# Kernel optimization log

Measured on AMD Instinct MI355X. Metric: run time of the kernel, lower is better.

The kernel has to match this reference:

```python
import jax, jax.numpy as jnp
import numpy as np

H = 64; H2 = 32; B = 256; NPART = 64
NP = B * NPART          # 16384 part nodes
PER_TF = 512            # torque/force nodes per graph
NT = B * PER_TF; NF = NT
E = 262144              # edges per edge type
L = 5; T = 4            # 4 main hetero layers + 1 actor layer; 4 edge types
NEG = 0.2; EPS = 1e-5


def _seg_softmax(e, seg, n):
    # softmax over entries sharing the same segment id (along axis 0)
    m = jax.lax.stop_gradient(jax.ops.segment_max(e, seg, num_segments=n))
    ex = jnp.exp(e - m[seg])
    s = jax.ops.segment_sum(ex, seg, num_segments=n)
    return ex / s[seg]


def _gat(x_s, x_d, es, ed, Ws, Wd, a_s, a_d, b, n_dst):
    # PyG GATConv, heads=1, add_self_loops=False, bipartite (x_src, x_dst)
    hs = x_s @ Ws                      # [Ns,H]
    hd = x_d @ Wd                      # [Nd,H]
    e = jax.nn.leaky_relu((hs @ a_s)[es] + (hd @ a_d)[ed], NEG)   # [E]
    al = _seg_softmax(e, ed, n_dst)                                # attn per dst neighborhood
    return jax.ops.segment_sum(al[:, None] * hs[es], ed, num_segments=n_dst) + b


def _hetero_layer(xp, xt, xf, edges, Ws, Wd, a_s, a_d, b):
    # to_hetero(aggr='sum'): one GATConv per edge type, sum into each dst type
    (pts, ptd), (tps, tpd), (pfs, pfd), (fps, fpd) = edges
    out_t = _gat(xp, xt, pts, ptd, Ws[0], Wd[0], a_s[0], a_d[0], b[0], xt.shape[0])
    out_p = (_gat(xt, xp, tps, tpd, Ws[1], Wd[1], a_s[1], a_d[1], b[1], xp.shape[0])
             + _gat(xf, xp, fps, fpd, Ws[3], Wd[3], a_s[3], a_d[3], b[3], xp.shape[0]))
    out_f = _gat(xp, xf, pfs, pfd, Ws[2], Wd[2], a_s[2], a_d[2], b[2], xf.shape[0])
    return out_p, out_t, out_f


def _pool(x):
    # MultiAggregation([max, min, mean]); segments are uniform -> reshape
    xr = x.reshape(B, -1, x.shape[-1])
    return jnp.concatenate([xr.max(1), xr.min(1), xr.mean(1)], axis=-1)


def reference(mass, part_state, torque_x, force_x,
              e_pt_src, e_pt_dst, e_tp_src, e_tp_dst,
              e_pf_src, e_pf_dst, e_fp_src, e_fp_dst,
              batch, part_id,
              emb_parts_W, emb_state, W_src, W_dst, a_src, a_dst, b_conv,
              ln_gamma, ln_beta, out_a_W, out_a_b,
              innet_W, innet_b, full_W, full_b, outnet_W, outnet_b):
    edges = ((e_pt_src, e_pt_dst), (e_tp_src, e_tp_dst),
             (e_pf_src, e_pf_dst), (e_fp_src, e_fp_dst))
    idx = part_state[:, 0] + 2 * part_state[:, 1]
    xp = jnp.concatenate([mass @ emb_parts_W, emb_state[idx]], axis=-1)  # [NP,H]
    xt, xf = torque_x, force_x
    for l in range(4):  # main hetero GAT, ReLU between layers, none after last
        xp, xt, xf = _hetero_layer(xp, xt, xf, edges,
                                   W_src[l], W_dst[l], a_src[l], a_dst[l], b_conv[l])
        if l < 3:
            xp, xt, xf = jax.nn.relu(xp), jax.nn.relu(xt), jax.nn.relu(xf)
    # actor: 1-layer hetero GAT (no activation)
    ap, at, af = _hetero_layer(xp, xt, xf, edges,
                               W_src[4], W_dst[4], a_src[4], a_dst[4], b_conv[4])
    # node LayerNorm
    mu = ap.mean(-1, keepdims=True)
    var = ((ap - mu) ** 2).mean(-1, keepdims=True)
    ra = (ap - mu) / jnp.sqrt(var + EPS) * ln_gamma + ln_beta
    ra = ra @ out_a_W + out_a_b                         # [NP,2]
    soft = _seg_softmax(ra, batch, B)                   # softmax per graph, per channel
    actions = jnp.zeros((B, 2, NPART), dtype=ra.dtype).at[batch, :, part_id].set(soft)
    actions = actions.reshape(B, 2 * NPART)
    rep = jnp.concatenate([_pool(xp), _pool(xt), _pool(xf)], axis=1)   # [B, 9H]
    repV = jax.nn.gelu(rep @ innet_W + innet_b, approximate=False)
    repV = jax.nn.gelu(repV @ full_W + full_b, approximate=False)
    V = jnp.tanh(repV @ outnet_W + outnet_b)            # [B,1]
    return actions, V


def setup_inputs():
    key = jax.random.key(0)
    ks = iter(jax.random.split(key, 40))
    f32 = jnp.float32
    inp = {}
    inp['mass'] = jax.random.uniform(next(ks), (NP, 1), dtype=f32)
    inp['part_state'] = jax.random.randint(next(ks), (NP, 2), 0, 2, dtype=jnp.int32)
    inp['torque_x'] = jax.random.normal(next(ks), (NT, H), dtype=f32)
    inp['force_x'] = jax.random.normal(next(ks), (NF, H), dtype=f32)
    for name, n in [('e_pt_src', NP), ('e_pt_dst', NT), ('e_tp_src', NT), ('e_tp_dst', NP),
                    ('e_pf_src', NP), ('e_pf_dst', NF), ('e_fp_src', NF), ('e_fp_dst', NP)]:
        inp[name] = jax.random.randint(next(ks), (E,), 0, n, dtype=jnp.int32)
    inp['batch'] = (jnp.arange(NP) // NPART).astype(jnp.int32)
    inp['part_id'] = (jnp.arange(NP) % NPART).astype(jnp.int32)
    s = 1.0 / np.sqrt(H)
    inp['emb_parts_W'] = jax.random.normal(next(ks), (1, H2), dtype=f32)
    inp['emb_state'] = jax.random.normal(next(ks), (4, H2), dtype=f32)
    inp['W_src'] = jax.random.normal(next(ks), (L, T, H, H), dtype=f32) * s
    inp['W_dst'] = jax.random.normal(next(ks), (L, T, H, H), dtype=f32) * s
    inp['a_src'] = jax.random.normal(next(ks), (L, T, H), dtype=f32) * s
    inp['a_dst'] = jax.random.normal(next(ks), (L, T, H), dtype=f32) * s
    inp['b_conv'] = jax.random.normal(next(ks), (L, T, H), dtype=f32) * 0.01
    inp['ln_gamma'] = jnp.ones((H,), dtype=f32)
    inp['ln_beta'] = jnp.zeros((H,), dtype=f32)
    inp['out_a_W'] = jax.random.normal(next(ks), (H, 2), dtype=f32) * s
    inp['out_a_b'] = jnp.zeros((2,), dtype=f32)
    inp['innet_W'] = jax.random.normal(next(ks), (9 * H, H), dtype=f32) / np.sqrt(9.0 * H)
    inp['innet_b'] = jnp.zeros((H,), dtype=f32)
    inp['full_W'] = jax.random.normal(next(ks), (H, H), dtype=f32) * s
    inp['full_b'] = jnp.zeros((H,), dtype=f32)
    inp['outnet_W'] = jax.random.normal(next(ks), (H, 1), dtype=f32) * s
    inp['outnet_b'] = jnp.zeros((1,), dtype=f32)
    return inp
```

## Files before the change

kernel.cpp:

```cpp
#include <hip/hip_runtime.h>
#include <math.h>

#define NP_ 16384
#define NT_ 131072
#define NF_ 131072
#define E_  262144
#define B_  256
#define NDTOT 294912
#define E4_  1048576

#define D0 0
#define D1 131072
#define D2 147456
#define D3 278528
#define S0 0
#define S1 16384
#define S2 147456
#define S3 163840

__device__ __forceinline__ float dot4(float4 a, float4 b) {
  return a.x * b.x + a.y * b.y + a.z * b.z + a.w * b.w;
}

__device__ __forceinline__ float4 gather_row(int kb, int ke, float ad,
    const int* __restrict__ sortsrc, const float* __restrict__ aS_seg,
    const float* __restrict__ xsrc, int q, int lanebase, float* si_out) {
  float4 acc = make_float4(0.f, 0.f, 0.f, 0.f);
  float m = -3e38f, ssum = 0.f;
  for (int base = kb; base < ke; base += 16) {
    int k = base + q;
    int valid = (k < ke);
    int sidx = valid ? sortsrc[k] : 0;
    float e = -3e38f;
    if (valid) {
      e = aS_seg[sidx] + ad;
      e = e > 0.f ? e : 0.2f * e;
    }
    float cm = e;
#pragma unroll
    for (int off = 1; off < 16; off <<= 1) cm = fmaxf(cm, __shfl_xor(cm, off));
    float mn = fmaxf(m, cm);
    float w = valid ? __expf(e - mn) : 0.f;
    float ws = w;
#pragma unroll
    for (int off = 1; off < 16; off <<= 1) ws += __shfl_xor(ws, off);
    float r = __expf(m - mn);
    ssum = ssum * r + ws;
    acc.x *= r; acc.y *= r; acc.z *= r; acc.w *= r;
    int cnt = min(16, ke - base);
    int i = 0;
    for (; i + 4 <= cnt; i += 4) {
      float w0 = __shfl(w, lanebase + i, 64);
      float w1 = __shfl(w, lanebase + i + 1, 64);
      float w2 = __shfl(w, lanebase + i + 2, 64);
      float w3 = __shfl(w, lanebase + i + 3, 64);
      int s0 = __shfl(sidx, lanebase + i, 64);
      int s1 = __shfl(sidx, lanebase + i + 1, 64);
      int s2 = __shfl(sidx, lanebase + i + 2, 64);
      int s3 = __shfl(sidx, lanebase + i + 3, 64);
      float4 x0 = *(const float4*)(xsrc + (size_t)s0 * 64 + q * 4);
      float4 x1 = *(const float4*)(xsrc + (size_t)s1 * 64 + q * 4);
      float4 x2 = *(const float4*)(xsrc + (size_t)s2 * 64 + q * 4);
      float4 x3 = *(const float4*)(xsrc + (size_t)s3 * 64 + q * 4);
      acc.x += w0 * x0.x + w1 * x1.x + w2 * x2.x + w3 * x3.x;
      acc.y += w0 * x0.y + w1 * x1.y + w2 * x2.y + w3 * x3.y;
      acc.z += w0 * x0.z + w1 * x1.z + w2 * x2.z + w3 * x3.z;
      acc.w += w0 * x0.w + w1 * x1.w + w2 * x2.w + w3 * x3.w;
    }
    for (; i < cnt; i++) {
      float wi = __shfl(w, lanebase + i, 64);
      int si = __shfl(sidx, lanebase + i, 64);
      float4 xv = *(const float4*)(xsrc + (size_t)si * 64 + q * 4);
      acc.x += wi * xv.x; acc.y += wi * xv.y; acc.z += wi * xv.z; acc.w += wi * xv.w;
    }
    m = mn;
  }
  *si_out = (ssum > 0.f) ? 1.f / ssum : 0.f;
  return acc;
}

__global__ void k_wa(const float* __restrict__ Wsrc, const float* __restrict__ Wdst,
                     const float* __restrict__ asrc, const float* __restrict__ adst,
                     float* __restrict__ wsas, float* __restrict__ wdad) {
  int b = blockIdx.x;
  int lt = b >> 1;
  int role = b & 1;
  int k = threadIdx.x;
  const float* W = (role == 0 ? Wsrc : Wdst) + ((size_t)(lt * 64 + k)) * 64;
  const float* a = (role == 0 ? asrc : adst) + lt * 64;
  float s = 0.f;
  for (int i = 0; i < 64; i++) s += W[i] * a[i];
  (role == 0 ? wsas : wdad)[lt * 64 + k] = s;
}

__global__ __launch_bounds__(256) void k_build_xp(const float* __restrict__ mass,
    const int* __restrict__ ps, const float* __restrict__ embW,
    const float* __restrict__ embS, const float* __restrict__ wsas,
    const float* __restrict__ wdad, float* __restrict__ xp,
    float* __restrict__ aS, float* __restrict__ aD) {
  int tid = threadIdx.x;
  int n = blockIdx.x * 16 + (tid >> 4);
  int q = tid & 15;
  float4 v;
  if (q < 8) {
    float mv = mass[n];
    const float* e = embW + q * 4;
    v.x = mv * e[0]; v.y = mv * e[1]; v.z = mv * e[2]; v.w = mv * e[3];
  } else {
    int idx = ps[n * 2] + 2 * ps[n * 2 + 1];
    const float4* e = (const float4*)(embS + idx * 32 + (q - 8) * 4);
    v = *e;
  }
  *(float4*)(xp + (size_t)n * 64 + q * 4) = v;
  float4 w0 = *(const float4*)(wsas + 0 * 64 + q * 4);
  float4 w2 = *(const float4*)(wsas + 2 * 64 + q * 4);
  float4 d1 = *(const float4*)(wdad + 1 * 64 + q * 4);
  float4 d3 = *(const float4*)(wdad + 3 * 64 + q * 4);
  float p0 = dot4(v, w0), p2 = dot4(v, w2), p1 = dot4(v, d1), p3 = dot4(v, d3);
#pragma unroll
  for (int off = 1; off < 16; off <<= 1) {
    p0 += __shfl_xor(p0, off); p2 += __shfl_xor(p2, off);
    p1 += __shfl_xor(p1, off); p3 += __shfl_xor(p3, off);
  }
  if (q == 0) { aS[S0 + n] = p0; aS[S2 + n] = p2; aD[D1 + n] = p1; aD[D3 + n] = p3; }
}

__global__ __launch_bounds__(256) void k_init_dots(const float* __restrict__ tx,
    const float* __restrict__ fx, const float* __restrict__ wsas,
    const float* __restrict__ wdad, float* __restrict__ aS, float* __restrict__ aD) {
  int tid = threadIdx.x;
  int q = tid & 15, slot = tid >> 4;
  int b = blockIdx.x;
  int isF = (b >= 8192);
  int n = (isF ? b - 8192 : b) * 16 + slot;
  const float* src = (isF ? fx : tx) + (size_t)n * 64 + q * 4;
  float4 v = *(const float4*)src;
  int tsrc = isF ? 3 : 1, tdst = isF ? 2 : 0;
  float4 ws = *(const float4*)(wsas + tsrc * 64 + q * 4);
  float4 wd = *(const float4*)(wdad + tdst * 64 + q * 4);
  float pS = dot4(v, ws), pD = dot4(v, wd);
#pragma unroll
  for (int off = 1; off < 16; off <<= 1) {
    pS += __shfl_xor(pS, off); pD += __shfl_xor(pD, off);
  }
  if (q == 0) {
    if (!isF) { aS[S1 + n] = pS; aD[D0 + n] = pD; }
    else      { aS[S3 + n] = pS; aD[D2 + n] = pD; }
  }
}

__global__ __launch_bounds__(256) void k_count(
    const int* __restrict__ d0, const int* __restrict__ d1,
    const int* __restrict__ d2, const int* __restrict__ d3,
    int* __restrict__ counts) {
  __shared__ int cnt[64];
  int b = blockIdx.x;
  int t = b >> 6, c = b & 63;
  const int* dp = (t == 0) ? d0 : (t == 1) ? d1 : (t == 2) ? d2 : d3;
  int sh = (t & 1) ? 8 : 11;
  int tid = threadIdx.x;
  if (tid < 64) cnt[tid] = 0;
  __syncthreads();
  const int4* dp4 = (const int4*)dp + (size_t)c * 1024;
  for (int i = tid; i < 1024; i += 256) {
    int4 v = dp4[i];
    atomicAdd(&cnt[v.x >> sh], 1);
    atomicAdd(&cnt[v.y >> sh], 1);
    atomicAdd(&cnt[v.z >> sh], 1);
    atomicAdd(&cnt[v.w >> sh], 1);
  }
  __syncthreads();
  if (tid < 64) counts[(b << 6) + tid] = cnt[tid];
}

__global__ __launch_bounds__(256) void k_bases(const int* __restrict__ counts,
    int* __restrict__ cbase, int* __restrict__ granBase, int* __restrict__ rowptr) {
  __shared__ int tot[256];
  int tid = threadIdx.x;
  int t = tid >> 6, g = tid & 63;
  int s = 0;
  for (int c = 0; c < 64; c++) s += counts[(((t << 6) | c) << 6) + g];
  tot[tid] = s;
  __syncthreads();
  for (int off = 1; off < 256; off <<= 1) {
    int x = 0; if (tid >= off) x = tot[tid - off];
    __syncthreads(); tot[tid] += x; __syncthreads();
  }
  int gb = tot[tid] - s;
  granBase[tid] = gb;
  if (tid == 255) granBase[256] = E4_;
  if (tid == 0) rowptr[NDTOT] = E4_;
  int run = gb;
  for (int c = 0; c < 64; c++) {
    int idx = (((t << 6) | c) << 6) + g;
    int v = counts[idx];
    cbase[idx] = run;
    run += v;
  }
}

__global__ __launch_bounds__(256) void k_place(
    const int* __restrict__ d0, const int* __restrict__ s0,
    const int* __restrict__ d1, const int* __restrict__ s1,
    const int* __restrict__ d2, const int* __restrict__ s2,
    const int* __restrict__ d3, const int* __restrict__ s3,
    const int* __restrict__ cbase, int2* __restrict__ pairs) {
  __shared__ int cur[64];
  int b = blockIdx.x;
  int t = b >> 6, c = b & 63;
  const int* dp; const int* sp;
  if (t == 0) { dp = d0; sp = s0; }
  else if (t == 1) { dp = d1; sp = s1; }
  else if (t == 2) { dp = d2; sp = s2; }
  else { dp = d3; sp = s3; }
  int sh = (t & 1) ? 8 : 11;
  int tid = threadIdx.x;
  if (tid < 64) cur[tid] = cbase[(b << 6) + tid];
  __syncthreads();
  const int4* dp4 = (const int4*)dp + (size_t)c * 1024;
  const int4* sp4 = (const int4*)sp + (size_t)c * 1024;
  for (int i = tid; i < 1024; i += 256) {
    int4 d = dp4[i];
    int4 s = sp4[i];
    int pos;
    pos = atomicAdd(&cur[d.x >> sh], 1); pairs[pos] = make_int2(d.x, s.x);
    pos = atomicAdd(&cur[d.y >> sh], 1); pairs[pos] = make_int2(d.y, s.y);
    pos = atomicAdd(&cur[d.z >> sh], 1); pairs[pos] = make_int2(d.z, s.z);
    pos = atomicAdd(&cur[d.w >> sh], 1); pairs[pos] = make_int2(d.w, s.w);
  }
}

__global__ __launch_bounds__(256) void k_build(const int2* __restrict__ pairs,
    const int* __restrict__ granBase, int* __restrict__ rowptr,
    int* __restrict__ sortsrc) {
  __shared__ int cnt[2048];
  __shared__ int psum[256];
  int g = blockIdx.x;
  int t = g >> 6, gg = g & 63;
  int rows = (t & 1) ? 256 : 2048;
  int rowLo = gg * rows;
  int csr0;
  if (t == 0) csr0 = D0 + rowLo;
  else if (t == 1) csr0 = D1 + rowLo;
  else if (t == 2) csr0 = D2 + rowLo;
  else csr0 = D3 + rowLo;
  int eb = granBase[g], ee = granBase[g + 1];
  int tid = threadIdx.x;
  for (int i = tid; i < rows; i += 256) cnt[i] = 0;
  __syncthreads();
  for (int i = eb + tid; i < ee; i += 256) {
    int2 p = pairs[i];
    atomicAdd(&cnt[p.x - rowLo], 1);
  }
  __syncthreads();
  int per = rows >> 8;
  int b0 = tid * per;
  int s = 0;
  for (int j = 0; j < per; j++) s += cnt[b0 + j];
  psum[tid] = s;
  __syncthreads();
  for (int off = 1; off < 256; off <<= 1) {
    int x = 0; if (tid >= off) x = psum[tid - off];
    __syncthreads(); psum[tid] += x; __syncthreads();
  }
  int run = psum[tid] - s;
  for (int j = 0; j < per; j++) {
    int v = cnt[b0 + j];
    cnt[b0 + j] = run;
    rowptr[csr0 + b0 + j] = eb + run;
    run += v;
  }
  __syncthreads();
  for (int i = eb + tid; i < ee; i += 256) {
    int2 p = pairs[i];
    int pos = eb + atomicAdd(&cnt[p.x - rowLo], 1);
    sortsrc[pos] = p.y;
  }
}

__global__ __launch_bounds__(256) void k_part_hs(int l, const float* __restrict__ Wsrc,
    const float* __restrict__ bconv, const float* __restrict__ xt,
    const float* __restrict__ xf, const float* __restrict__ xp,
    const int* __restrict__ rowptr, const int* __restrict__ sortsrc,
    const float* __restrict__ aSrd, const float* __restrict__ aDrd,
    float* __restrict__ aSwr, float* __restrict__ aDwr,
    const float* __restrict__ wsas, const float* __restrict__ wdad,
    float* __restrict__ xpo, float* __restrict__ hs0, float* __restrict__ hs2,
    int relu, int writeDots) {
  __shared__ float Wl[4096];
  __shared__ float shC[2176];
  int tid = threadIdx.x;

  if (blockIdx.x >= NP_ / 16) {
    int b = blockIdx.x - NP_ / 16;
    const float4* W0g = (const float4*)(Wsrc + (size_t)(l * 4 + 0) * 4096);
    const float4* W2g = (const float4*)(Wsrc + (size_t)(l * 4 + 2) * 4096);
#pragma unroll
    for (int i = 0; i < 4; i++) ((float4*)Wl)[i * 256 + tid] = W0g[i * 256 + tid];
    int rlocal = tid >> 4, q = tid & 15;
    int n = b * 16 + rlocal;
    float4 xv = *(const float4*)(xp + (size_t)n * 64 + q * 4);
    *(float4*)(shC + rlocal * 68 + q * 4) = xv;
    __syncthreads();
    const float* xr = shC + rlocal * 68;
    const float4* Wc = (const float4*)Wl;
    float4 o0 = make_float4(0.f, 0.f, 0.f, 0.f);
#pragma unroll 4
    for (int k4 = 0; k4 < 16; k4++) {
      float4 a4 = *(const float4*)(xr + k4 * 4);
#pragma unroll
      for (int kk = 0; kk < 4; kk++) {
        float av = kk == 0 ? a4.x : kk == 1 ? a4.y : kk == 2 ? a4.z : a4.w;
        float4 w0 = Wc[(k4 * 4 + kk) * 16 + q];
        o0.x += av * w0.x; o0.y += av * w0.y; o0.z += av * w0.z; o0.w += av * w0.w;
      }
    }
    *(float4*)(hs0 + (size_t)n * 64 + q * 4) = o0;
    __syncthreads();
#pragma unroll
    for (int i = 0; i < 4; i++) ((float4*)Wl)[i * 256 + tid] = W2g[i * 256 + tid];
    __syncthreads();
    float4 o2 = make_float4(0.f, 0.f, 0.f, 0.f);
#pragma unroll 4
    for (int k4 = 0; k4 < 16; k4++) {
      float4 a4 = *(const float4*)(xr + k4 * 4);
#pragma unroll
      for (int kk = 0; kk < 4; kk++) {
        float av = kk == 0 ? a4.x : kk == 1 ? a4.y : kk == 2 ? a4.z : a4.w;
        float4 w2 = Wc[(k4 * 4 + kk) * 16 + q];
        o2.x += av * w2.x; o2.y += av * w2.y; o2.z += av * w2.z; o2.w += av * w2.w;
      }
    }
    *(float4*)(hs2 + (size_t)n * 64 + q * 4) = o2;
    return;
  }

  float* rowA = shC; float* rowB = shC + 1088;
  const float4* W1g = (const float4*)(Wsrc + (size_t)(l * 4 + 1) * 4096);
  const float4* W3g = (const float4*)(Wsrc + (size_t)(l * 4 + 3) * 4096);
#pragma unroll
  for (int i = 0; i < 4; i++) ((float4*)Wl)[i * 256 + tid] = W1g[i * 256 + tid];

  int rlocal = tid >> 4;
  int q = tid & 15;
  int lanebase = (tid & 63) & 48;
  int n = blockIdx.x * 16 + rlocal;
  int row1 = D1 + n;
  int row3 = D3 + n;

  {
    int kb = rowptr[row1], ke = rowptr[row1 + 1];
    float si;
    float4 acc = gather_row(kb, ke, aDrd[row1], sortsrc, aSrd + S1, xt, q, lanebase, &si);
    acc.x *= si; acc.y *= si; acc.z *= si; acc.w *= si;
    *(float4*)(rowA + rlocal * 68 + q * 4) = acc;
  }
  {
    int kb = rowptr[row3], ke = rowptr[row3 + 1];
    float si;
    float4 acc = gather_row(kb, ke, aDrd[row3], sortsrc, aSrd + S3, xf, q, lanebase, &si);
    acc.x *= si; acc.y *= si; acc.z *= si; acc.w *= si;
    *(float4*)(rowB + rlocal * 68 + q * 4) = acc;
  }
  __syncthreads();

  const float* b1 = bconv + (l * 4 + 1) * 64;
  const float* b3 = bconv + (l * 4 + 3) * 64;
  float4 o = *(const float4*)(b1 + q * 4);
  float4 o3b = *(const float4*)(b3 + q * 4);
  o.x += o3b.x; o.y += o3b.y; o.z += o3b.z; o.w += o3b.w;
  const float4* Wc = (const float4*)Wl;
#pragma unroll 4
  for (int k4 = 0; k4 < 16; k4++) {
    float4 a4 = *(const float4*)(rowA + rlocal * 68 + k4 * 4);
#pragma unroll
    for (int kk = 0; kk < 4; kk++) {
      float av = kk == 0 ? a4.x : kk == 1 ? a4.y : kk == 2 ? a4.z : a4.w;
      float4 w1 = Wc[(k4 * 4 + kk) * 16 + q];
      o.x += av * w1.x; o.y += av * w1.y; o.z += av * w1.z; o.w += av * w1.w;
    }
  }
  __syncthreads();
#pragma unroll
  for (int i = 0; i < 4; i++) ((float4*)Wl)[i * 256 + tid] = W3g[i * 256 + tid];
  __syncthreads();
#pragma unroll 4
  for (int k4 = 0; k4 < 16; k4++) {
    float4 b4 = *(const float4*)(rowB + rlocal * 68 + k4 * 4);
#pragma unroll
    for (int kk = 0; kk < 4; kk++) {
      float bv = kk == 0 ? b4.x : kk == 1 ? b4.y : kk == 2 ? b4.z : b4.w;
      float4 w3 = Wc[(k4 * 4 + kk) * 16 + q];
      o.x += bv * w3.x; o.y += bv * w3.y; o.z += bv * w3.z; o.w += bv * w3.w;
    }
  }
  if (relu) { o.x = fmaxf(o.x, 0.f); o.y = fmaxf(o.y, 0.f); o.z = fmaxf(o.z, 0.f); o.w = fmaxf(o.w, 0.f); }
  *(float4*)(xpo + (size_t)n * 64 + q * 4) = o;

  if (writeDots) {
    float4 w0 = *(const float4*)(wsas + (size_t)((l + 1) * 4 + 0) * 64 + q * 4);
    float4 w2 = *(const float4*)(wsas + (size_t)((l + 1) * 4 + 2) * 64 + q * 4);
    float4 d1 = *(const float4*)(wdad + (size_t)((l + 1) * 4 + 1) * 64 + q * 4);
    float4 d3 = *(const float4*)(wdad + (size_t)((l + 1) * 4 + 3) * 64 + q * 4);
    float p0 = dot4(o, w0), p2 = dot4(o, w2), p1 = dot4(o, d1), p3 = dot4(o, d3);
#pragma unroll
    for (int off = 1; off < 16; off <<= 1) {
      p0 += __shfl_xor(p0, off); p2 += __shfl_xor(p2, off);
      p1 += __shfl_xor(p1, off); p3 += __shfl_xor(p3, off);
    }
    if (q == 0) { aSwr[S0 + n] = p0; aSwr[S2 + n] = p2; aDwr[D1 + n] = p1; aDwr[D3 + n] = p3; }
  }
}

__global__ __launch_bounds__(256) void k_tf(int l, const float* __restrict__ hs0,
    const float* __restrict__ hs2, const float* __restrict__ bconv,
    const int* __restrict__ rowptr, const int* __restrict__ sortsrc,
    const float* __restrict__ aSrd, const float* __restrict__ aDrd,
    float* __restrict__ aSwr, float* __restrict__ aDwr,
    const float* __restrict__ wsas, const float* __restrict__ wdad,
    float* __restrict__ xt, float* __restrict__ xf, int relu) {
  int tid = threadIdx.x;
  int q = tid & 15, slot = tid >> 4;
  int lanebase = (tid & 63) & 48;
  int b = blockIdx.x;
  int isF = (b >= 8192);
  int rg = ((isF ? b - 8192 : b) * 16 + slot);
  int csr = (isF ? D2 : D0) + rg;
  const float* hs = isF ? hs2 : hs0;
  const float* aSseg = aSrd + (isF ? S2 : S0);
  int t = isF ? 2 : 0;

  int kb = rowptr[csr], ke = rowptr[csr + 1];
  float si;
  float4 acc = gather_row(kb, ke, aDrd[csr], sortsrc, aSseg, hs, q, lanebase, &si);
  float4 bias = *(const float4*)(bconv + (size_t)(l * 4 + t) * 64 + q * 4);
  float4 o;
  o.x = acc.x * si + bias.x; o.y = acc.y * si + bias.y;
  o.z = acc.z * si + bias.z; o.w = acc.w * si + bias.w;
  if (relu) {
    o.x = fmaxf(o.x, 0.f); o.y = fmaxf(o.y, 0.f);
    o.z = fmaxf(o.z, 0.f); o.w = fmaxf(o.w, 0.f);
  }
  *(float4*)((isF ? xf : xt) + (size_t)rg * 64 + q * 4) = o;

  int tsrc = isF ? 3 : 1, tdst = isF ? 2 : 0;
  float4 wsv = *(const float4*)(wsas + (size_t)((l + 1) * 4 + tsrc) * 64 + q * 4);
  float4 wdv = *(const float4*)(wdad + (size_t)((l + 1) * 4 + tdst) * 64 + q * 4);
  float pS = dot4(o, wsv);
  float pD = dot4(o, wdv);
#pragma unroll
  for (int off = 1; off < 16; off <<= 1) {
    pS += __shfl_xor(pS, off); pD += __shfl_xor(pD, off);
  }
  if (q == 0) {
    if (!isF) { aSwr[S1 + rg] = pS; aDwr[D0 + rg] = pD; }
    else      { aSwr[S3 + rg] = pS; aDwr[D2 + rg] = pD; }
  }
}

__global__ __launch_bounds__(256) void k_actor(const float* __restrict__ ap,
    const float* __restrict__ gamma, const float* __restrict__ beta,
    const float* __restrict__ oaW, const float* __restrict__ oab,
    float* __restrict__ outp) {
  __shared__ float r0s[64], r1s[64];
  int g = blockIdx.x;
  int wave = threadIdx.x >> 6, lane = threadIdx.x & 63;
  float gl = gamma[lane], bl = beta[lane];
  float w0 = oaW[lane * 2], w1 = oaW[lane * 2 + 1];
  float ob0 = oab[0], ob1 = oab[1];
  for (int i = 0; i < 16; i++) {
    int n = g * 64 + wave * 16 + i;
    float v = ap[(size_t)n * 64 + lane];
    float s = v;
    for (int off = 32; off > 0; off >>= 1) s += __shfl_xor(s, off);
    float mean = s * (1.f / 64.f);
    float d = v - mean;
    float s2 = d * d;
    for (int off = 32; off > 0; off >>= 1) s2 += __shfl_xor(s2, off);
    float var = s2 * (1.f / 64.f);
    float y = d / sqrtf(var + 1e-5f) * gl + bl;
    float p0 = y * w0, p1 = y * w1;
    for (int off = 32; off > 0; off >>= 1) { p0 += __shfl_xor(p0, off); p1 += __shfl_xor(p1, off); }
    if (lane == 0) { r0s[wave * 16 + i] = p0 + ob0; r1s[wave * 16 + i] = p1 + ob1; }
  }
  __syncthreads();
  if (threadIdx.x < 64) {
    int p = threadIdx.x;
    float r0 = r0s[p], r1 = r1s[p];
    float m0 = r0, m1 = r1;
    for (int off = 32; off > 0; off >>= 1) {
      m0 = fmaxf(m0, __shfl_xor(m0, off));
      m1 = fmaxf(m1, __shfl_xor(m1, off));
    }
    float e0 = __expf(r0 - m0), e1 = __expf(r1 - m1);
    float s0 = e0, s1 = e1;
    for (int off = 32; off > 0; off >>= 1) { s0 += __shfl_xor(s0, off); s1 += __shfl_xor(s1, off); }
    outp[g * 128 + p] = e0 / s0;
    outp[g * 128 + 64 + p] = e1 / s1;
  }
}

__global__ __launch_bounds__(256) void k_pool(const float* __restrict__ xp,
    const float* __restrict__ xt, const float* __restrict__ xf,
    float* __restrict__ pool) {
  __shared__ float pmax[4][64], pmin[4][64], psum[4][64];
  int b = blockIdx.x;
  int g = b / 9, c = b % 9;
  int tid = threadIdx.x;
  int grp = tid >> 6, col = tid & 63;
  const float* src; int R;
  if (c == 0)      { src = xp + (size_t)g * 64 * 64; R = 64; }
  else if (c <= 4) { src = xt + ((size_t)g * 512 + (size_t)(c - 1) * 128) * 64; R = 128; }
  else             { src = xf + ((size_t)g * 512 + (size_t)(c - 5) * 128) * 64; R = 128; }
  float mx = -3e38f, mn = 3e38f, sm = 0.f;
  for (int r = grp; r < R; r += 4) {
    float v = src[(size_t)r * 64 + col];
    mx = fmaxf(mx, v); mn = fminf(mn, v); sm += v;
  }
  pmax[grp][col] = mx; pmin[grp][col] = mn; psum[grp][col] = sm;
  __syncthreads();
  if (grp == 0) {
    float M = fmaxf(fmaxf(pmax[0][col], pmax[1][col]), fmaxf(pmax[2][col], pmax[3][col]));
    float m = fminf(fminf(pmin[0][col], pmin[1][col]), fminf(pmin[2][col], pmin[3][col]));
    float S = psum[0][col] + psum[1][col] + psum[2][col] + psum[3][col];
    float* o = pool + ((size_t)(g * 9 + c) * 3) * 64;
    o[col] = M; o[64 + col] = m; o[128 + col] = S;
  }
}

__global__ __launch_bounds__(256) void k_vhead(const float* __restrict__ pool,
    const float* __restrict__ inW, const float* __restrict__ inb,
    const float* __restrict__ fW, const float* __restrict__ fb,
    const float* __restrict__ oW, const float* __restrict__ ob,
    float* __restrict__ outV) {
  __shared__ float rep[576];
  __shared__ float red[256];
  __shared__ float h1[64];
  int g = blockIdx.x, tid = threadIdx.x;
  if (tid < 64) {
    int col = tid;
    const float* pg = pool + (size_t)g * 9 * 3 * 64;
    rep[col] = pg[col];
    rep[64 + col] = pg[64 + col];
    rep[128 + col] = pg[128 + col] * (1.f / 64.f);
    float M = -3e38f, m = 3e38f, S = 0.f;
    for (int c = 1; c <= 4; c++) {
      const float* p = pg + (size_t)c * 192;
      M = fmaxf(M, p[col]); m = fminf(m, p[64 + col]); S += p[128 + col];
    }
    rep[192 + col] = M; rep[256 + col] = m; rep[320 + col] = S * (1.f / 512.f);
    M = -3e38f; m = 3e38f; S = 0.f;
    for (int c = 5; c <= 8; c++) {
      const float* p = pg + (size_t)c * 192;
      M = fmaxf(M, p[col]); m = fminf(m, p[64 + col]); S += p[128 + col];
    }
    rep[384 + col] = M; rep[448 + col] = m; rep[512 + col] = S * (1.f / 512.f);
  }
  __syncthreads();
  const float ISQ2 = 0.70710678118654752f;
  {
    int j = tid & 63, p = tid >> 6;
    float s = 0.f;
    for (int k = p * 144; k < (p + 1) * 144; k++) s += rep[k] * inW[k * 64 + j];
    red[tid] = s;
  }
  __syncthreads();
  if (tid < 64) {
    float s = red[tid] + red[64 + tid] + red[128 + tid] + red[192 + tid] + inb[tid];
    h1[tid] = 0.5f * s * (1.f + erff(s * ISQ2));
  }
  __syncthreads();
  if (tid < 64) {
    float s = fb[tid];
    for (int k = 0; k < 64; k++) s += h1[k] * fW[k * 64 + tid];
    float h2 = 0.5f * s * (1.f + erff(s * ISQ2));
    float p = h2 * oW[tid];
    for (int off = 32; off > 0; off >>= 1) p += __shfl_xor(p, off);
    if (tid == 0) outV[g] = tanhf(p + ob[0]);
  }
}

extern "C" void kernel_launch(void* const* d_in, const int* in_sizes, int n_in,
                              void* d_out, int out_size, void* d_ws, size_t ws_size,
                              hipStream_t stream) {
  (void)in_sizes; (void)n_in; (void)out_size; (void)ws_size;
  const float* mass = (const float*)d_in[0];
  const int*   ps   = (const int*)d_in[1];
  const float* torque_x = (const float*)d_in[2];
  const float* force_x  = (const float*)d_in[3];
  const int* ept_s = (const int*)d_in[4];  const int* ept_d = (const int*)d_in[5];
  const int* etp_s = (const int*)d_in[6];  const int* etp_d = (const int*)d_in[7];
  const int* epf_s = (const int*)d_in[8];  const int* epf_d = (const int*)d_in[9];
  const int* efp_s = (const int*)d_in[10]; const int* efp_d = (const int*)d_in[11];
  const float* embW  = (const float*)d_in[14];
  const float* embS  = (const float*)d_in[15];
  const float* Wsrc  = (const float*)d_in[16];
  const float* Wdst  = (const float*)d_in[17];
  const float* asrc  = (const float*)d_in[18];
  const float* adst  = (const float*)d_in[19];
  const float* bconv = (const float*)d_in[20];
  const float* gamma = (const float*)d_in[21];
  const float* beta  = (const float*)d_in[22];
  const float* oaW   = (const float*)d_in[23];
  const float* oab   = (const float*)d_in[24];
  const float* inW   = (const float*)d_in[25];
  const float* inb   = (const float*)d_in[26];
  const float* fW    = (const float*)d_in[27];
  const float* fb    = (const float*)d_in[28];
  const float* oW    = (const float*)d_in[29];
  const float* ob    = (const float*)d_in[30];

  char* base = (char*)d_ws;
  size_t off = 0;
  auto alloc = [&](size_t bytes) -> void* {
    void* r = base + off;
    off = (off + bytes + 255) & ~(size_t)255;
    return r;
  };
  float* xp0 = (float*)alloc((size_t)NP_ * 64 * 4);
  float* xp1 = (float*)alloc((size_t)NP_ * 64 * 4);
  float* xt  = (float*)alloc((size_t)NT_ * 64 * 4);
  float* xf  = (float*)alloc((size_t)NF_ * 64 * 4);
  float* hs0 = (float*)alloc((size_t)NP_ * 64 * 4);
  float* hs2 = (float*)alloc((size_t)NP_ * 64 * 4);
  float* aSb[2], *aDb[2];
  aSb[0] = (float*)alloc((size_t)NDTOT * 4);
  aSb[1] = (float*)alloc((size_t)NDTOT * 4);
  aDb[0] = (float*)alloc((size_t)NDTOT * 4);
  aDb[1] = (float*)alloc((size_t)NDTOT * 4);
  float* wsas = (float*)alloc(1280 * 4);
  float* wdad = (float*)alloc(1280 * 4);
  float* pool = (float*)alloc((size_t)B_ * 9 * 3 * 64 * 4);
  int* rowptr = (int*)alloc((size_t)(NDTOT + 1) * 4);
  int* sortsrc = (int*)alloc((size_t)E4_ * 4);
  int2* pairs  = (int2*)alloc((size_t)E4_ * 8);
  int* counts  = (int*)alloc(16384 * 4);
  int* cbase   = (int*)alloc(16384 * 4);
  int* granBase = (int*)alloc(257 * 4);

  k_wa<<<40, 64, 0, stream>>>(Wsrc, Wdst, asrc, adst, wsas, wdad);
  k_build_xp<<<NP_ / 16, 256, 0, stream>>>(mass, ps, embW, embS, wsas, wdad,
                                           xp0, aSb[0], aDb[0]);
  k_init_dots<<<(NT_ + NF_) / 16, 256, 0, stream>>>(torque_x, force_x,
                                                    wsas, wdad, aSb[0], aDb[0]);
  k_count<<<256, 256, 0, stream>>>(ept_d, etp_d, epf_d, efp_d, counts);
  k_bases<<<1, 256, 0, stream>>>(counts, cbase, granBase, rowptr);
  k_place<<<256, 256, 0, stream>>>(ept_d, ept_s, etp_d, etp_s, epf_d, epf_s,
                                   efp_d, efp_s, cbase, pairs);
  k_build<<<256, 256, 0, stream>>>(pairs, granBase, rowptr, sortsrc);

  float* xpbuf[2] = { xp0, xp1 };
  int cur = 0;
  for (int l = 0; l < 5; l++) {
    int ri = l & 1, wi = (l + 1) & 1;
    int relu = (l < 3) ? 1 : 0;
    const float* xtr = (l == 0) ? torque_x : xt;
    const float* xfr = (l == 0) ? force_x : xf;
    int grid = (l < 4) ? (2 * NP_ / 16) : (NP_ / 16);
    k_part_hs<<<grid, 256, 0, stream>>>(l, Wsrc, bconv, xtr, xfr, xpbuf[cur],
                                        rowptr, sortsrc,
                                        aSb[ri], aDb[ri], aSb[wi], aDb[wi],
                                        wsas, wdad, xpbuf[1 - cur], hs0, hs2,
                                        relu, (l < 4) ? 1 : 0);
    if (l < 4)
      k_tf<<<(NT_ + NF_) / 16, 256, 0, stream>>>(l, hs0, hs2, bconv, rowptr, sortsrc,
                                                 aSb[ri], aDb[ri], aSb[wi], aDb[wi],
                                                 wsas, wdad, xt, xf, relu);
    cur = 1 - cur;
  }

  float* outp = (float*)d_out;
  k_actor<<<B_, 256, 0, stream>>>(xp1, gamma, beta, oaW, oab, outp);
  k_pool<<<B_ * 9, 256, 0, stream>>>(xp0, xt, xf, pool);
  k_vhead<<<B_, 256, 0, stream>>>(pool, inW, inb, fW, fb, oW, ob, outp + B_ * 128);
}
```

Before: 579.8 us.

## Interleave two neighbor gathers per thread and fuse actor LayerNorm head

Replaces the single-row softmax gather with one that walks two destination rows at once, so each thread keeps twice as many independent row loads in flight. The part kernel uses it for the torque and force aggregations, and the torque/force kernel now handles two rows per thread group with half the blocks. The last layer's LayerNorm and actor projection move into the part kernel epilogue, so k_actor only runs the per-graph softmax over precomputed logits. Costs are more register pressure, lower occupancy and wasted work when the two rows have different degrees.

```diff
diff --git a/kernel.cpp b/kernel.cpp
--- a/kernel.cpp
+++ b/kernel.cpp
@@ -22,61 +22,87 @@
   return a.x * b.x + a.y * b.y + a.z * b.z + a.w * b.w;
 }
 
-__device__ __forceinline__ float4 gather_row(int kb, int ke, float ad,
-    const int* __restrict__ sortsrc, const float* __restrict__ aS_seg,
-    const float* __restrict__ xsrc, int q, int lanebase, float* si_out) {
-  float4 acc = make_float4(0.f, 0.f, 0.f, 0.f);
-  float m = -3e38f, ssum = 0.f;
-  for (int base = kb; base < ke; base += 16) {
-    int k = base + q;
-    int valid = (k < ke);
-    int sidx = valid ? sortsrc[k] : 0;
-    float e = -3e38f;
-    if (valid) {
-      e = aS_seg[sidx] + ad;
-      e = e > 0.f ? e : 0.2f * e;
-    }
-    float cm = e;
-#pragma unroll
-    for (int off = 1; off < 16; off <<= 1) cm = fmaxf(cm, __shfl_xor(cm, off));
-    float mn = fmaxf(m, cm);
-    float w = valid ? __expf(e - mn) : 0.f;
-    float ws = w;
-#pragma unroll
-    for (int off = 1; off < 16; off <<= 1) ws += __shfl_xor(ws, off);
-    float r = __expf(m - mn);
-    ssum = ssum * r + ws;
-    acc.x *= r; acc.y *= r; acc.z *= r; acc.w *= r;
-    int cnt = min(16, ke - base);
-    int i = 0;
-    for (; i + 4 <= cnt; i += 4) {
-      float w0 = __shfl(w, lanebase + i, 64);
-      float w1 = __shfl(w, lanebase + i + 1, 64);
-      float w2 = __shfl(w, lanebase + i + 2, 64);
-      float w3 = __shfl(w, lanebase + i + 3, 64);
-      int s0 = __shfl(sidx, lanebase + i, 64);
-      int s1 = __shfl(sidx, lanebase + i + 1, 64);
-      int s2 = __shfl(sidx, lanebase + i + 2, 64);
-      int s3 = __shfl(sidx, lanebase + i + 3, 64);
-      float4 x0 = *(const float4*)(xsrc + (size_t)s0 * 64 + q * 4);
-      float4 x1 = *(const float4*)(xsrc + (size_t)s1 * 64 + q * 4);
-      float4 x2 = *(const float4*)(xsrc + (size_t)s2 * 64 + q * 4);
-      float4 x3 = *(const float4*)(xsrc + (size_t)s3 * 64 + q * 4);
-      acc.x += w0 * x0.x + w1 * x1.x + w2 * x2.x + w3 * x3.x;
-      acc.y += w0 * x0.y + w1 * x1.y + w2 * x2.y + w3 * x3.y;
-      acc.z += w0 * x0.z + w1 * x1.z + w2 * x2.z + w3 * x3.z;
-      acc.w += w0 * x0.w + w1 * x1.w + w2 * x2.w + w3 * x3.w;
-    }
-    for (; i < cnt; i++) {
-      float wi = __shfl(w, lanebase + i, 64);
-      int si = __shfl(sidx, lanebase + i, 64);
-      float4 xv = *(const float4*)(xsrc + (size_t)si * 64 + q * 4);
-      acc.x += wi * xv.x; acc.y += wi * xv.y; acc.z += wi * xv.z; acc.w += wi * xv.w;
-    }
-    m = mn;
-  }
-  *si_out = (ssum > 0.f) ? 1.f / ssum : 0.f;
-  return acc;
+__device__ __forceinline__ void gather2(
+    int kb0, int ke0, float ad0, const float* __restrict__ aS0, const float* __restrict__ x0,
+    int kb1, int ke1, float ad1, const float* __restrict__ aS1, const float* __restrict__ x1,
+    const int* __restrict__ sortsrc, int q, int lanebase,
+    float4* __restrict__ acc0o, float* __restrict__ si0o,
+    float4* __restrict__ acc1o, float* __restrict__ si1o) {
+  float4 acc0 = make_float4(0.f, 0.f, 0.f, 0.f);
+  float4 acc1 = make_float4(0.f, 0.f, 0.f, 0.f);
+  float m0 = -3e38f, m1 = -3e38f, sum0 = 0.f, sum1 = 0.f;
+  int len = max(ke0 - kb0, ke1 - kb1);
+  for (int c = 0; c < len; c += 16) {
+    int k0 = kb0 + c + q, k1 = kb1 + c + q;
+    int v0 = k0 < ke0, v1 = k1 < ke1;
+    int sx0 = v0 ? sortsrc[k0] : 0;
+    int sx1 = v1 ? sortsrc[k1] : 0;
+    float e0 = -3e38f, e1 = -3e38f;
+    if (v0) { float t = aS0[sx0] + ad0; e0 = t > 0.f ? t : 0.2f * t; }
+    if (v1) { float t = aS1[sx1] + ad1; e1 = t > 0.f ? t : 0.2f * t; }
+    float cm0 = e0, cm1 = e1;
+#pragma unroll
+    for (int off = 1; off < 16; off <<= 1) {
+      cm0 = fmaxf(cm0, __shfl_xor(cm0, off));
+      cm1 = fmaxf(cm1, __shfl_xor(cm1, off));
+    }
+    float mn0 = fmaxf(m0, cm0), mn1 = fmaxf(m1, cm1);
+    float w0 = v0 ? __expf(e0 - mn0) : 0.f;
+    float w1 = v1 ? __expf(e1 - mn1) : 0.f;
+    float ws0 = w0, ws1 = w1;
+#pragma unroll
+    for (int off = 1; off < 16; off <<= 1) {
+      ws0 += __shfl_xor(ws0, off);
+      ws1 += __shfl_xor(ws1, off);
+    }
+    float r0 = __expf(m0 - mn0), r1 = __expf(m1 - mn1);
+    sum0 = sum0 * r0 + ws0;
+    sum1 = sum1 * r1 + ws1;
+    acc0.x *= r0; acc0.y *= r0; acc0.z *= r0; acc0.w *= r0;
+    acc1.x *= r1; acc1.y *= r1; acc1.z *= r1; acc1.w *= r1;
+    int cnt0 = ke0 - (kb0 + c); cnt0 = cnt0 < 0 ? 0 : (cnt0 > 16 ? 16 : cnt0);
+    int cnt1 = ke1 - (kb1 + c); cnt1 = cnt1 < 0 ? 0 : (cnt1 > 16 ? 16 : cnt1);
+    int cmax = max(cnt0, cnt1);
+    for (int i = 0; i < cmax; i += 4) {
+      float wa0 = __shfl(w0, lanebase + i, 64);
+      float wa1 = __shfl(w0, lanebase + i + 1, 64);
+      float wa2 = __shfl(w0, lanebase + i + 2, 64);
+      float wa3 = __shfl(w0, lanebase + i + 3, 64);
+      int sa0 = __shfl(sx0, lanebase + i, 64);
+      int sa1 = __shfl(sx0, lanebase + i + 1, 64);
+      int sa2 = __shfl(sx0, lanebase + i + 2, 64);
+      int sa3 = __shfl(sx0, lanebase + i + 3, 64);
+      float wb0 = __shfl(w1, lanebase + i, 64);
+      float wb1 = __shfl(w1, lanebase + i + 1, 64);
+      float wb2 = __shfl(w1, lanebase + i + 2, 64);
+      float wb3 = __shfl(w1, lanebase + i + 3, 64);
+      int sb0 = __shfl(sx1, lanebase + i, 64);
+      int sb1 = __shfl(sx1, lanebase + i + 1, 64);
+      int sb2 = __shfl(sx1, lanebase + i + 2, 64);
+      int sb3 = __shfl(sx1, lanebase + i + 3, 64);
+      float4 xa0 = *(const float4*)(x0 + (size_t)sa0 * 64 + q * 4);
+      float4 xa1 = *(const float4*)(x0 + (size_t)sa1 * 64 + q * 4);
+      float4 xa2 = *(const float4*)(x0 + (size_t)sa2 * 64 + q * 4);
+      float4 xa3 = *(const float4*)(x0 + (size_t)sa3 * 64 + q * 4);
+      float4 xb0 = *(const float4*)(x1 + (size_t)sb0 * 64 + q * 4);
+      float4 xb1 = *(const float4*)(x1 + (size_t)sb1 * 64 + q * 4);
+      float4 xb2 = *(const float4*)(x1 + (size_t)sb2 * 64 + q * 4);
+      float4 xb3 = *(const float4*)(x1 + (size_t)sb3 * 64 + q * 4);
+      acc0.x += wa0 * xa0.x + wa1 * xa1.x + wa2 * xa2.x + wa3 * xa3.x;
+      acc0.y += wa0 * xa0.y + wa1 * xa1.y + wa2 * xa2.y + wa3 * xa3.y;
+      acc0.z += wa0 * xa0.z + wa1 * xa1.z + wa2 * xa2.z + wa3 * xa3.z;
+      acc0.w += wa0 * xa0.w + wa1 * xa1.w + wa2 * xa2.w + wa3 * xa3.w;
+      acc1.x += wb0 * xb0.x + wb1 * xb1.x + wb2 * xb2.x + wb3 * xb3.x;
+      acc1.y += wb0 * xb0.y + wb1 * xb1.y + wb2 * xb2.y + wb3 * xb3.y;
+      acc1.z += wb0 * xb0.z + wb1 * xb1.z + wb2 * xb2.z + wb3 * xb3.z;
+      acc1.w += wb0 * xb0.w + wb1 * xb1.w + wb2 * xb2.w + wb3 * xb3.w;
+    }
+    m0 = mn0; m1 = mn1;
+  }
+  *si0o = (sum0 > 0.f) ? 1.f / sum0 : 0.f;
+  *si1o = (sum1 > 0.f) ? 1.f / sum1 : 0.f;
+  *acc0o = acc0;
+  *acc1o = acc1;
 }
 
 __global__ void k_wa(const float* __restrict__ Wsrc, const float* __restrict__ Wdst,
@@ -286,7 +312,10 @@
     float* __restrict__ aSwr, float* __restrict__ aDwr,
     const float* __restrict__ wsas, const float* __restrict__ wdad,
     float* __restrict__ xpo, float* __restrict__ hs0, float* __restrict__ hs2,
-    int relu, int writeDots) {
+    int relu, int writeDots,
+    const float* __restrict__ gamma, const float* __restrict__ beta,
+    const float* __restrict__ oaW, const float* __restrict__ oab,
+    float* __restrict__ raOut) {
   __shared__ float Wl[4096];
   __shared__ float shC[2176];
   int tid = threadIdx.x;
@@ -349,18 +378,16 @@
   int row3 = D3 + n;
 
   {
-    int kb = rowptr[row1], ke = rowptr[row1 + 1];
-    float si;
-    float4 acc = gather_row(kb, ke, aDrd[row1], sortsrc, aSrd + S1, xt, q, lanebase, &si);
-    acc.x *= si; acc.y *= si; acc.z *= si; acc.w *= si;
-    *(float4*)(rowA + rlocal * 68 + q * 4) = acc;
-  }
-  {
-    int kb = rowptr[row3], ke = rowptr[row3 + 1];
-    float si;
-    float4 acc = gather_row(kb, ke, aDrd[row3], sortsrc, aSrd + S3, xf, q, lanebase, &si);
-    acc.x *= si; acc.y *= si; acc.z *= si; acc.w *= si;
-    *(float4*)(rowB + rlocal * 68 + q * 4) = acc;
+    int kb1 = rowptr[row1], ke1 = rowptr[row1 + 1];
+    int kb3 = rowptr[row3], ke3 = rowptr[row3 + 1];
+    float4 accA, accB; float siA, siB;
+    gather2(kb1, ke1, aDrd[row1], aSrd + S1, xt,
+            kb3, ke3, aDrd[row3], aSrd + S3, xf,
+            sortsrc, q, lanebase, &accA, &siA, &accB, &siB);
+    accA.x *= siA; accA.y *= siA; accA.z *= siA; accA.w *= siA;
+    accB.x *= siB; accB.y *= siB; accB.z *= siB; accB.w *= siB;
+    *(float4*)(rowA + rlocal * 68 + q * 4) = accA;
+    *(float4*)(rowB + rlocal * 68 + q * 4) = accB;
   }
   __syncthreads();
 
@@ -394,6 +421,39 @@
       o.x += bv * w3.x; o.y += bv * w3.y; o.z += bv * w3.z; o.w += bv * w3.w;
     }
   }
+
+  if (raOut) {
+    float ssum = o.x + o.y + o.z + o.w;
+#pragma unroll
+    for (int off = 1; off < 16; off <<= 1) ssum += __shfl_xor(ssum, off);
+    float mean = ssum * (1.f / 64.f);
+    float dx = o.x - mean, dy = o.y - mean, dz = o.z - mean, dw = o.w - mean;
+    float v2 = dx * dx + dy * dy + dz * dz + dw * dw;
+#pragma unroll
+    for (int off = 1; off < 16; off <<= 1) v2 += __shfl_xor(v2, off);
+    float rstd = 1.f / sqrtf(v2 * (1.f / 64.f) + 1e-5f);
+    float4 g4 = *(const float4*)(gamma + q * 4);
+    float4 be4 = *(const float4*)(beta + q * 4);
+    float y0 = dx * rstd * g4.x + be4.x;
+    float y1 = dy * rstd * g4.y + be4.y;
+    float y2 = dz * rstd * g4.z + be4.z;
+    float y3 = dw * rstd * g4.w + be4.w;
+    float4 wA = *(const float4*)(oaW + q * 8);
+    float4 wB = *(const float4*)(oaW + q * 8 + 4);
+    float p0 = y0 * wA.x + y1 * wA.z + y2 * wB.x + y3 * wB.z;
+    float p1 = y0 * wA.y + y1 * wA.w + y2 * wB.y + y3 * wB.w;
+#pragma unroll
+    for (int off = 1; off < 16; off <<= 1) {
+      p0 += __shfl_xor(p0, off);
+      p1 += __shfl_xor(p1, off);
+    }
+    if (q == 0) {
+      raOut[(size_t)n * 2]     = p0 + oab[0];
+      raOut[(size_t)n * 2 + 1] = p1 + oab[1];
+    }
+    return;
+  }
+
   if (relu) { o.x = fmaxf(o.x, 0.f); o.y = fmaxf(o.y, 0.f); o.z = fmaxf(o.z, 0.f); o.w = fmaxf(o.w, 0.f); }
   *(float4*)(xpo + (size_t)n * 64 + q * 4) = o;
 
@@ -423,81 +483,77 @@
   int q = tid & 15, slot = tid >> 4;
   int lanebase = (tid & 63) & 48;
   int b = blockIdx.x;
-  int isF = (b >= 8192);
-  int rg = ((isF ? b - 8192 : b) * 16 + slot);
-  int csr = (isF ? D2 : D0) + rg;
+  int isF = (b >= 4096);
+  int rg0 = (isF ? b - 4096 : b) * 32 + slot;
+  int rg1 = rg0 + 16;
+  int csr0 = (isF ? D2 : D0) + rg0;
+  int csr1 = csr0 + 16;
   const float* hs = isF ? hs2 : hs0;
   const float* aSseg = aSrd + (isF ? S2 : S0);
   int t = isF ? 2 : 0;
 
-  int kb = rowptr[csr], ke = rowptr[csr + 1];
-  float si;
-  float4 acc = gather_row(kb, ke, aDrd[csr], sortsrc, aSseg, hs, q, lanebase, &si);
+  int kb0 = rowptr[csr0], ke0 = rowptr[csr0 + 1];
+  int kb1 = rowptr[csr1], ke1 = rowptr[csr1 + 1];
+  float4 acc0, acc1; float si0, si1;
+  gather2(kb0, ke0, aDrd[csr0], aSseg, hs,
+          kb1, ke1, aDrd[csr1], aSseg, hs,
+          sortsrc, q, lanebase, &acc0, &si0, &acc1, &si1);
+
   float4 bias = *(const float4*)(bconv + (size_t)(l * 4 + t) * 64 + q * 4);
-  float4 o;
-  o.x = acc.x * si + bias.x; o.y = acc.y * si + bias.y;
-  o.z = acc.z * si + bias.z; o.w = acc.w * si + bias.w;
+  float4 o0, o1;
+  o0.x = acc0.x * si0 + bias.x; o0.y = acc0.y * si0 + bias.y;
+  o0.z = acc0.z * si0 + bias.z; o0.w = acc0.w * si0 + bias.w;
+  o1.x = acc1.x * si1 + bias.x; o1.y = acc1.y * si1 + bias.y;
+  o1.z = acc1.z * si1 + bias.z; o1.w = acc1.w * si1 + bias.w;
   if (relu) {
-    o.x = fmaxf(o.x, 0.f); o.y = fmaxf(o.y, 0.f);
-    o.z = fmaxf(o.z, 0.f); o.w = fmaxf(o.w, 0.f);
-  }
-  *(float4*)((isF ? xf : xt) + (size_t)rg * 64 + q * 4) = o;
+    o0.x = fmaxf(o0.x, 0.f); o0.y = fmaxf(o0.y, 0.f);
+    o0.z = fmaxf(o0.z, 0.f); o0.w = fmaxf(o0.w, 0.f);
+    o1.x = fmaxf(o1.x, 0.f); o1.y = fmaxf(o1.y, 0.f);
+    o1.z = fmaxf(o1.z, 0.f); o1.w = fmaxf(o1.w, 0.f);
+  }
+  float* xout = isF ? xf : xt;
+  *(float4*)(xout + (size_t)rg0 * 64 + q * 4) = o0;
+  *(float4*)(xout + (size_t)rg1 * 64 + q * 4) = o1;
 
   int tsrc = isF ? 3 : 1, tdst = isF ? 2 : 0;
   float4 wsv = *(const float4*)(wsas + (size_t)((l + 1) * 4 + tsrc) * 64 + q * 4);
   float4 wdv = *(const float4*)(wdad + (size_t)((l + 1) * 4 + tdst) * 64 + q * 4);
-  float pS = dot4(o, wsv);
-  float pD = dot4(o, wdv);
+  float pS0 = dot4(o0, wsv), pD0 = dot4(o0, wdv);
+  float pS1 = dot4(o1, wsv), pD1 = dot4(o1, wdv);
 #pragma unroll
   for (int off = 1; off < 16; off <<= 1) {
-    pS += __shfl_xor(pS, off); pD += __shfl_xor(pD, off);
+    pS0 += __shfl_xor(pS0, off); pD0 += __shfl_xor(pD0, off);
+    pS1 += __shfl_xor(pS1, off); pD1 += __shfl_xor(pD1, off);
   }
   if (q == 0) {
-    if (!isF) { aSwr[S1 + rg] = pS; aDwr[D0 + rg] = pD; }
-    else      { aSwr[S3 + rg] = pS; aDwr[D2 + rg] = pD; }
-  }
-}
-
-__global__ __launch_bounds__(256) void k_actor(const float* __restrict__ ap,
-    const float* __restrict__ gamma, const float* __restrict__ beta,
-    const float* __restrict__ oaW, const float* __restrict__ oab,
-    float* __restrict__ outp) {
-  __shared__ float r0s[64], r1s[64];
+    if (!isF) {
+      aSwr[S1 + rg0] = pS0; aDwr[D0 + rg0] = pD0;
+      aSwr[S1 + rg1] = pS1; aDwr[D0 + rg1] = pD1;
+    } else {
+      aSwr[S3 + rg0] = pS0; aDwr[D2 + rg0] = pD0;
+      aSwr[S3 + rg1] = pS1; aDwr[D2 + rg1] = pD1;
+    }
+  }
+}
+
+__global__ __launch_bounds__(64) void k_actor(const float* __restrict__ ra,
+                                              float* __restrict__ outp) {
   int g = blockIdx.x;
-  int wave = threadIdx.x >> 6, lane = threadIdx.x & 63;
-  float gl = gamma[lane], bl = beta[lane];
-  float w0 = oaW[lane * 2], w1 = oaW[lane * 2 + 1];
-  float ob0 = oab[0], ob1 = oab[1];
-  for (int i = 0; i < 16; i++) {
-    int n = g * 64 + wave * 16 + i;
-    float v = ap[(size_t)n * 64 + lane];
-    float s = v;
-    for (int off = 32; off > 0; off >>= 1) s += __shfl_xor(s, off);
-    float mean = s * (1.f / 64.f);
-    float d = v - mean;
-    float s2 = d * d;
-    for (int off = 32; off > 0; off >>= 1) s2 += __shfl_xor(s2, off);
-    float var = s2 * (1.f / 64.f);
-    float y = d / sqrtf(var + 1e-5f) * gl + bl;
-    float p0 = y * w0, p1 = y * w1;
-    for (int off = 32; off > 0; off >>= 1) { p0 += __shfl_xor(p0, off); p1 += __shfl_xor(p1, off); }
-    if (lane == 0) { r0s[wave * 16 + i] = p0 + ob0; r1s[wave * 16 + i] = p1 + ob1; }
-  }
-  __syncthreads();
-  if (threadIdx.x < 64) {
-    int p = threadIdx.x;
-    float r0 = r0s[p], r1 = r1s[p];
-    float m0 = r0, m1 = r1;
-    for (int off = 32; off > 0; off >>= 1) {
-      m0 = fmaxf(m0, __shfl_xor(m0, off));
-      m1 = fmaxf(m1, __shfl_xor(m1, off));
-    }
-    float e0 = __expf(r0 - m0), e1 = __expf(r1 - m1);
-    float s0 = e0, s1 = e1;
-    for (int off = 32; off > 0; off >>= 1) { s0 += __shfl_xor(s0, off); s1 += __shfl_xor(s1, off); }
-    outp[g * 128 + p] = e0 / s0;
-    outp[g * 128 + 64 + p] = e1 / s1;
-  }
+  int p = threadIdx.x;
+  float2 rv = *(const float2*)(ra + (size_t)(g * 64 + p) * 2);
+  float m0 = rv.x, m1 = rv.y;
+  for (int off = 32; off > 0; off >>= 1) {
+    m0 = fmaxf(m0, __shfl_xor(m0, off));
+    m1 = fmaxf(m1, __shfl_xor(m1, off));
+  }
+  float e0 = __expf(rv.x - m0), e1 = __expf(rv.y - m1);
+  float s0 = e0, s1 = e1;
+  for (int off = 32; off > 0; off >>= 1) {
+    s0 += __shfl_xor(s0, off);
+    s1 += __shfl_xor(s1, off);
+  }
+  outp[g * 128 + p] = e0 / s0;
+  outp[g * 128 + 64 + p] = e1 / s1;
 }
 
 __global__ __launch_bounds__(256) void k_pool(const float* __restrict__ xp,
@@ -631,6 +687,7 @@
   float* wsas = (float*)alloc(1280 * 4);
   float* wdad = (float*)alloc(1280 * 4);
   float* pool = (float*)alloc((size_t)B_ * 9 * 3 * 64 * 4);
+  float* ra   = (float*)alloc((size_t)NP_ * 2 * 4);
   int* rowptr = (int*)alloc((size_t)(NDTOT + 1) * 4);
   int* sortsrc = (int*)alloc((size_t)E4_ * 4);
   int2* pairs  = (int2*)alloc((size_t)E4_ * 8);
@@ -661,16 +718,18 @@
                                         rowptr, sortsrc,
                                         aSb[ri], aDb[ri], aSb[wi], aDb[wi],
                                         wsas, wdad, xpbuf[1 - cur], hs0, hs2,
-                                        relu, (l < 4) ? 1 : 0);
+                                        relu, (l < 4) ? 1 : 0,
+                                        gamma, beta, oaW, oab,
+                                        (l == 4) ? ra : (float*)nullptr);
     if (l < 4)
-      k_tf<<<(NT_ + NF_) / 16, 256, 0, stream>>>(l, hs0, hs2, bconv, rowptr, sortsrc,
+      k_tf<<<(NT_ + NF_) / 32, 256, 0, stream>>>(l, hs0, hs2, bconv, rowptr, sortsrc,
                                                  aSb[ri], aDb[ri], aSb[wi], aDb[wi],
                                                  wsas, wdad, xt, xf, relu);
     cur = 1 - cur;
   }
 
   float* outp = (float*)d_out;
-  k_actor<<<B_, 256, 0, stream>>>(xp1, gamma, beta, oaW, oab, outp);
+  k_actor<<<B_, 64, 0, stream>>>(ra, outp);
   k_pool<<<B_ * 9, 256, 0, stream>>>(xp0, xt, xf, pool);
   k_vhead<<<B_, 256, 0, stream>>>(pool, inW, inb, fW, fb, oW, ob, outp + B_ * 128);
 }
```

New measurement: 552.5 us. -4.7%, faster.
